# Kernel tuning notes

Measured on AMD Instinct MI355X. Metric: run time of the kernel, lower is better.

The kernel has to match this reference:

```python
import jax, jax.numpy as jnp
import numpy as np

D_MODEL = 1024
HEADS = 16
HEAD_DIM = D_MODEL // HEADS
SEQ_LEN = 2048
BATCH = 2
LN_EPS = 1e-5


def _layernorm(x, gamma, beta):
    mu = jnp.mean(x, axis=-1, keepdims=True)
    var = jnp.var(x, axis=-1, keepdims=True)
    return (x - mu) * jax.lax.rsqrt(var + LN_EPS) * gamma + beta


def setup_inputs() -> dict:
    key = jax.random.key(0)
    ks = jax.random.split(key, 12)
    d, h = D_MODEL, 4 * D_MODEL
    s = lambda fan_in: 1.0 / np.sqrt(fan_in)
    return {
        "x": jax.random.normal(ks[0], (BATCH, SEQ_LEN, d), dtype=jnp.float32),
        "W_qkv": jax.random.uniform(ks[1], (d, 3 * d), minval=-s(d), maxval=s(d)),
        "b_qkv": jax.random.uniform(ks[2], (3 * d,), minval=-s(d), maxval=s(d)),
        "W1": jax.random.uniform(ks[3], (d, h), minval=-s(d), maxval=s(d)),
        "b1": jax.random.uniform(ks[4], (h,), minval=-s(d), maxval=s(d)),
        "W2": jax.random.uniform(ks[5], (h, d), minval=-s(h), maxval=s(h)),
        "b2": jax.random.uniform(ks[6], (d,), minval=-s(h), maxval=s(h)),
        "ln1_g": jnp.ones((d,), jnp.float32),
        "ln1_b": jnp.zeros((d,), jnp.float32),
        "ln2_g": jnp.ones((d,), jnp.float32),
        "ln2_b": jnp.zeros((d,), jnp.float32),
    }


def reference(x, W_qkv, b_qkv, W1, b1, W2, b2, ln1_g, ln1_b, ln2_g, ln2_b):
    B, T, C = x.shape
    # QKV projection -> [B, T, 3, H, hs] -> q,k,v each [B, H, T, hs]
    qkv = (x @ W_qkv + b_qkv).reshape(B, T, 3, HEADS, HEAD_DIM)
    qkv = jnp.transpose(qkv, (2, 0, 3, 1, 4))
    q, k, v = qkv[0], qkv[1], qkv[2]
    # Naive causal attention with full [B,H,T,T] score matrix (matches source)
    A = jnp.einsum("bhqd,bhkd->bhqk", q, k) / jnp.sqrt(jnp.float32(HEAD_DIM))
    causal = jnp.tril(jnp.ones((T, T), dtype=bool))
    A = jnp.where(causal, A, -jnp.inf)
    A = jax.nn.softmax(A, axis=-1)
    attn = jnp.einsum("bhqk,bhkd->bhqd", A, v)  # [B,H,T,hs]
    attn = jnp.transpose(attn, (0, 2, 1, 3)).reshape(B, T, C)
    # Residual + LN, FFN, residual + LN (dropout=0 / eval)
    h = _layernorm(x + attn, ln1_g, ln1_b)
    ff = jax.nn.relu(h @ W1 + b1) @ W2 + b2
    return _layernorm(h + ff, ln2_g, ln2_b)
```

## Files before the change

### kernel.cpp

```cpp
#include <hip/hip_runtime.h>

#define D_MODEL 1024
#define HEADS   16
#define HEAD_DIM 64
#define SEQ     2048
#define BATCH   2
#define ROWS    (BATCH*SEQ)
#define FFDIM   4096

typedef __attribute__((ext_vector_type(8))) short short8;
typedef __attribute__((ext_vector_type(4))) float f32x4;
typedef __attribute__((ext_vector_type(4))) unsigned short us4;

typedef const __attribute__((address_space(1))) unsigned int* gptr_t;
typedef __attribute__((address_space(3))) unsigned int* lptr_t;

__device__ __forceinline__ unsigned short f2bf(float f){
  unsigned int x = __float_as_uint(f);
  x += 0x7fffu + ((x >> 16) & 1u);
  return (unsigned short)(x >> 16);
}

__device__ __forceinline__ float wave_sum(float x){
  #pragma unroll
  for (int off = 32; off; off >>= 1) x += __shfl_xor(x, off);
  return x;
}

__global__ __launch_bounds__(256) void cast_bf16_kernel(const float* __restrict__ in,
                                                        unsigned short* __restrict__ out, int n4){
  int i = blockIdx.x * 256 + threadIdx.x;
  if (i >= n4) return;
  float4 v = *(const float4*)(in + (size_t)i * 4);
  us4 o;
  o[0] = f2bf(v.x); o[1] = f2bf(v.y); o[2] = f2bf(v.z); o[3] = f2bf(v.w);
  *(us4*)(out + (size_t)i * 4) = o;
}

__global__ __launch_bounds__(256) void transpose_cast_kernel(const float* __restrict__ in,
                                                             unsigned short* __restrict__ out,
                                                             int R, int C){
  __shared__ float tile[32][33];
  const int bc = blockIdx.x * 32, br = blockIdx.y * 32;
  const int tx = threadIdx.x & 31, ty = threadIdx.x >> 5;
  #pragma unroll
  for (int j = 0; j < 4; ++j)
    tile[ty + 8*j][tx] = in[(size_t)(br + ty + 8*j) * C + bc + tx];
  __syncthreads();
  #pragma unroll
  for (int j = 0; j < 4; ++j)
    out[(size_t)(bc + ty + 8*j) * R + br + tx] = f2bf(tile[tx][ty + 8*j]);
}

template<int EPI>
__global__ __launch_bounds__(256) void gemm_kernel(const unsigned short* __restrict__ A,
                                                   const unsigned short* __restrict__ BT,
                                                   const float* __restrict__ bias,
                                                   int M, int N, int K, int kchunk,
                                                   int gx, int gy,
                                                   float* __restrict__ outF,
                                                   unsigned short* __restrict__ outH,
                                                   unsigned short* __restrict__ qo,
                                                   unsigned short* __restrict__ ko,
                                                   unsigned short* __restrict__ vT){
  __shared__ __align__(16) unsigned short Alds[2][128 * 32];
  __shared__ __align__(16) unsigned short Blds[2][128 * 32];
  const int tid = threadIdx.x;
  const int lane = tid & 63;
  const int wid = tid >> 6;
  const int wr = wid >> 1, wc = wid & 1;
  const int lrow = lane & 15, lgrp = lane >> 4;

  const int nwg = gridDim.x;
  const int cpx = nwg >> 3;
  const int wg = (blockIdx.x & 7) * cpx + (blockIdx.x >> 3);
  const int nx = wg % gx;
  const int rest = wg / gx;
  const int my = rest % gy;
  const int sk = rest / gy;

  const int m0 = my * 128, n0 = nx * 128;
  const int kbase0 = sk * kchunk;

  const int sr = lane >> 2, sc = (lane & 3) * 8;

  f32x4 acc[4][4];
  #pragma unroll
  for (int i = 0; i < 4; ++i)
    #pragma unroll
    for (int j = 0; j < 4; ++j)
      acc[i][j] = f32x4{0.f, 0.f, 0.f, 0.f};

  #pragma unroll
  for (int it = 0; it < 2; ++it){
    const int c = wid * 2 + it;
    const int r = c * 16 + sr;
    __builtin_amdgcn_global_load_lds(
        (gptr_t)(const void*)(A + (size_t)(m0 + r) * K + kbase0 + sc),
        (lptr_t)(void*)(&Alds[0][c * 512]), 16, 0, 0);
    __builtin_amdgcn_global_load_lds(
        (gptr_t)(const void*)(BT + (size_t)(n0 + r) * K + kbase0 + sc),
        (lptr_t)(void*)(&Blds[0][c * 512]), 16, 0, 0);
  }

  const int nk = kchunk >> 5;
  int cur = 0;
  for (int kt = 0; kt < nk; ++kt){
    __syncthreads();

    if (kt + 1 < nk){
      const int kb = kbase0 + (kt + 1) * 32;
      #pragma unroll
      for (int it = 0; it < 2; ++it){
        const int c = wid * 2 + it;
        const int r = c * 16 + sr;
        __builtin_amdgcn_global_load_lds(
            (gptr_t)(const void*)(A + (size_t)(m0 + r) * K + kb + sc),
            (lptr_t)(void*)(&Alds[cur ^ 1][c * 512]), 16, 0, 0);
        __builtin_amdgcn_global_load_lds(
            (gptr_t)(const void*)(BT + (size_t)(n0 + r) * K + kb + sc),
            (lptr_t)(void*)(&Blds[cur ^ 1][c * 512]), 16, 0, 0);
      }
    }

    short8 af[4], bfr[4];
    #pragma unroll
    for (int f = 0; f < 4; ++f){
      af[f]  = *(const short8*)&Alds[cur][(wr * 64 + f * 16 + lrow) * 32 + lgrp * 8];
      bfr[f] = *(const short8*)&Blds[cur][(wc * 64 + f * 16 + lrow) * 32 + lgrp * 8];
    }
    __builtin_amdgcn_s_setprio(1);
    #pragma unroll
    for (int i = 0; i < 4; ++i)
      #pragma unroll
      for (int j = 0; j < 4; ++j)
        acc[i][j] = __builtin_amdgcn_mfma_f32_16x16x32_bf16(af[i], bfr[j], acc[i][j], 0, 0, 0);
    __builtin_amdgcn_s_setprio(0);
    cur ^= 1;
  }

  float* const outP = (EPI == 3) ? outF + (size_t)sk * M * N : outF;
  #pragma unroll
  for (int i = 0; i < 4; ++i){
    const int rg = m0 + wr * 64 + i * 16 + lgrp * 4;
    #pragma unroll
    for (int j = 0; j < 4; ++j){
      const int cg = n0 + wc * 64 + j * 16 + lrow;
      const float bb = (EPI == 3) ? 0.f : bias[cg];
      if constexpr (EPI == 0){
        const int which = cg >> 10, rem = cg & 1023;
        const int hh = rem >> 6, dd = rem & 63;
        const int bb_ = rg >> 11, tt = rg & 2047;
        const size_t bh = (size_t)(bb_ * HEADS + hh);
        if (which == 2){
          us4 pk;
          #pragma unroll
          for (int r = 0; r < 4; ++r) pk[r] = f2bf(acc[i][j][r] + bb);
          *(us4*)(vT + (bh * 64 + dd) * SEQ + tt) = pk;
        } else {
          unsigned short* dst = which ? ko : qo;
          const float sc2 = which ? 1.0f : 0.18033688f;
          #pragma unroll
          for (int r = 0; r < 4; ++r)
            dst[(bh * SEQ + tt + r) * 64 + dd] = f2bf((acc[i][j][r] + bb) * sc2);
        }
      } else if constexpr (EPI == 1){
        #pragma unroll
        for (int r = 0; r < 4; ++r)
          outH[(size_t)(rg + r) * N + cg] = f2bf(fmaxf(acc[i][j][r] + bb, 0.f));
      } else {
        #pragma unroll
        for (int r = 0; r < 4; ++r)
          outP[(size_t)(rg + r) * N + cg] = acc[i][j][r] + bb;
      }
    }
  }
}

__global__ __launch_bounds__(512, 2) void gemm256_kernel(const unsigned short* __restrict__ A,
                                                         const unsigned short* __restrict__ BT,
                                                         const float* __restrict__ bias,
                                                         int M, int N, int K, int gx,
                                                         unsigned short* __restrict__ outH){
  __shared__ __align__(16) unsigned short Al[2][256 * 32];
  __shared__ __align__(16) unsigned short Bl[2][256 * 32];
  const int tid = threadIdx.x;
  const int lane = tid & 63;
  const int wid = tid >> 6;
  const int wm = wid >> 2, wn = wid & 3;
  const int lr = lane & 15, g = lane >> 4;

  const int nwg = gridDim.x;
  const int cpx = nwg >> 3;
  const int wg = (blockIdx.x & 7) * cpx + (blockIdx.x >> 3);
  const int nx = wg % gx, my = wg / gx;
  const int m0 = my * 256, n0 = nx * 256;

  f32x4 acc[8][4];
  #pragma unroll
  for (int i = 0; i < 8; ++i)
    #pragma unroll
    for (int j = 0; j < 4; ++j)
      acc[i][j] = f32x4{0.f, 0.f, 0.f, 0.f};

  auto STAGE = [&](int buf, int kt){
    const int kb = kt * 32;
    #pragma unroll
    for (int j = 0; j < 2; ++j){
      const int cc = tid + j * 512;
      const int row = cc >> 2, c = cc & 3;
      const int scol = ((c ^ (row & 3)) << 3);
      __builtin_amdgcn_global_load_lds(
          (gptr_t)(const void*)(A + (size_t)(m0 + row) * K + kb + scol),
          (lptr_t)(void*)(&Al[buf][cc * 8]), 16, 0, 0);
      __builtin_amdgcn_global_load_lds(
          (gptr_t)(const void*)(BT + (size_t)(n0 + row) * K + kb + scol),
          (lptr_t)(void*)(&Bl[buf][cc * 8]), 16, 0, 0);
    }
  };

  const int nk = K >> 5;
  STAGE(0, 0);
  for (int t = 0; t < nk; ++t){
    const int buf = t & 1;
    __syncthreads();
    if (t + 1 < nk) STAGE(buf ^ 1, t + 1);

    short8 af[8], bf[4];
    #pragma unroll
    for (int i = 0; i < 8; ++i){
      const int row = wm * 128 + i * 16 + lr;
      af[i] = *(const short8*)&Al[buf][row * 32 + ((g * 8) ^ ((row & 3) << 3))];
    }
    #pragma unroll
    for (int j = 0; j < 4; ++j){
      const int row = wn * 64 + j * 16 + lr;
      bf[j] = *(const short8*)&Bl[buf][row * 32 + ((g * 8) ^ ((row & 3) << 3))];
    }
    __builtin_amdgcn_s_setprio(1);
    #pragma unroll
    for (int i = 0; i < 8; ++i)
      #pragma unroll
      for (int j = 0; j < 4; ++j)
        acc[i][j] = __builtin_amdgcn_mfma_f32_16x16x32_bf16(af[i], bf[j], acc[i][j], 0, 0, 0);
    __builtin_amdgcn_s_setprio(0);
  }

  #pragma unroll
  for (int i = 0; i < 8; ++i){
    const int rg = m0 + wm * 128 + i * 16 + g * 4;
    #pragma unroll
    for (int j = 0; j < 4; ++j){
      const int cg = n0 + wn * 64 + j * 16 + lr;
      const float bb = bias[cg];
      #pragma unroll
      for (int r = 0; r < 4; ++r)
        outH[(size_t)(rg + r) * N + cg] = f2bf(fmaxf(acc[i][j][r] + bb, 0.f));
    }
  }
}

__global__ __launch_bounds__(256) void attn_mfma_kernel(const unsigned short* __restrict__ Qb,
                                                        const unsigned short* __restrict__ Kb,
                                                        const unsigned short* __restrict__ VT,
                                                        float* __restrict__ Op){
  __shared__ __align__(16) char Kl[2][8192];
  __shared__ __align__(16) char Vl[2][8192];
  __shared__ __align__(16) char Pl[4][4096];
  const int tid = threadIdx.x;
  const int w = tid >> 6, lane = tid & 63;
  const int lr = lane & 15, g = lane >> 4;

  const int bx = blockIdx.x, u = bx & 255, half = bx >> 8;
  const int g8 = u >> 5;
  const int qg = half ? g8 : 15 - g8;
  const int bh = u & 31;

  const int q0w = qg * 128 + w * 32;
  const int qA = q0w + lr, qB = qA + 16;

  const char* const KbB = (const char*)(Kb + (size_t)bh * SEQ * 64);
  const char* const VbB = (const char*)(VT + (size_t)bh * 64 * SEQ);
  char* const PbA = Pl[w];
  char* const PbB = Pl[w] + 2048;

  const unsigned short* qra = Qb + ((size_t)bh * SEQ + qA) * 64 + g * 8;
  const short8 qfA0 = *(const short8*)(qra);
  const short8 qfA1 = *(const short8*)(qra + 32);
  const short8 qfB0 = *(const short8*)(qra + 16 * 64);
  const short8 qfB1 = *(const short8*)(qra + 16 * 64 + 32);

  f32x4 oA[4], oB[4];
  #pragma unroll
  for (int dt = 0; dt < 4; ++dt){ oA[dt] = f32x4{0.f,0.f,0.f,0.f}; oB[dt] = f32x4{0.f,0.f,0.f,0.f}; }
  float lA = 0.f, lB = 0.f;
  const int swzl = (lr & 7) << 4;

  const int kbmax = 2 * qg + 1;

  short8 st[4];
  {
    #pragma unroll
    for (int c = 0; c < 2; ++c){
      const int L = c * 4096 + tid * 16;
      st[c] = *(const short8*)(KbB + L);
      const int row = L >> 7, col = L & 127;
      st[2 + c] = *(const short8*)(VbB + (size_t)row * 4096 + col);
    }
  }

  for (int kb = 0; kb <= kbmax; ++kb){
    const int p = kb & 1;
    const int k0 = kb * 64;

    #pragma unroll
    for (int c = 0; c < 2; ++c){
      const int L = c * 4096 + tid * 16;
      const int row = L >> 7, col = L & 127;
      const int dst = row * 128 + (col ^ ((row & 7) << 4));
      *(short8*)(Kl[p] + dst) = st[c];
      *(short8*)(Vl[p] + dst) = st[2 + c];
    }
    __syncthreads();

    if (kb < kbmax){
      #pragma unroll
      for (int c = 0; c < 2; ++c){
        const int L = c * 4096 + tid * 16;
        st[c] = *(const short8*)(KbB + (size_t)(kb + 1) * 8192 + L);
        const int row = L >> 7, col = L & 127;
        st[2 + c] = *(const short8*)(VbB + (size_t)row * 4096 + (size_t)(kb + 1) * 128 + col);
      }
    }

    f32x4 sA[4], sB[4];
    __builtin_amdgcn_s_setprio(1);
    #pragma unroll
    for (int kt = 0; kt < 4; ++kt){
      const int row = kt * 16 + lr;
      const int ro = row * 128, sw = (row & 7) << 4;
      const short8 kf0 = *(const short8*)(Kl[p] + ro + ((g * 16) ^ sw));
      const short8 kf1 = *(const short8*)(Kl[p] + ro + ((64 + g * 16) ^ sw));
      sA[kt] = __builtin_amdgcn_mfma_f32_16x16x32_bf16(kf0, qfA0, f32x4{0.f,0.f,0.f,0.f}, 0, 0, 0);
      sA[kt] = __builtin_amdgcn_mfma_f32_16x16x32_bf16(kf1, qfA1, sA[kt], 0, 0, 0);
      sB[kt] = __builtin_amdgcn_mfma_f32_16x16x32_bf16(kf0, qfB0, f32x4{0.f,0.f,0.f,0.f}, 0, 0, 0);
      sB[kt] = __builtin_amdgcn_mfma_f32_16x16x32_bf16(kf1, qfB1, sB[kt], 0, 0, 0);
    }
    __builtin_amdgcn_s_setprio(0);

    if (kb >= kbmax - 1){
      #pragma unroll
      for (int kt = 0; kt < 4; ++kt)
        #pragma unroll
        for (int r = 0; r < 4; ++r){
          const int key = k0 + kt * 16 + g * 4 + r;
          if (key > qA) sA[kt][r] = -INFINITY;
          if (key > qB) sB[kt][r] = -INFINITY;
        }
    }

    {
      float sum = 0.f;
      #pragma unroll
      for (int kt = 0; kt < 4; ++kt){
        #pragma unroll
        for (int r = 0; r < 4; ++r){
          const float pp = __builtin_amdgcn_exp2f(sA[kt][r]);
          sA[kt][r] = pp; sum += pp;
        }
        unsigned int p01, p23;
        asm("v_cvt_pk_bf16_f32 %0, %1, %2" : "=v"(p01) : "v"(sA[kt][0]), "v"(sA[kt][1]));
        asm("v_cvt_pk_bf16_f32 %0, %1, %2" : "=v"(p23) : "v"(sA[kt][2]), "v"(sA[kt][3]));
        uint2 pk; pk.x = p01; pk.y = p23;
        *(uint2*)(PbA + lr * 128 + ((kt * 32 + g * 8) ^ swzl)) = pk;
      }
      sum += __shfl_xor(sum, 16);
      sum += __shfl_xor(sum, 32);
      lA += sum;
    }
    {
      float sum = 0.f;
      #pragma unroll
      for (int kt = 0; kt < 4; ++kt){
        #pragma unroll
        for (int r = 0; r < 4; ++r){
          const float pp = __builtin_amdgcn_exp2f(sB[kt][r]);
          sB[kt][r] = pp; sum += pp;
        }
        unsigned int p01, p23;
        asm("v_cvt_pk_bf16_f32 %0, %1, %2" : "=v"(p01) : "v"(sB[kt][0]), "v"(sB[kt][1]));
        asm("v_cvt_pk_bf16_f32 %0, %1, %2" : "=v"(p23) : "v"(sB[kt][2]), "v"(sB[kt][3]));
        uint2 pk; pk.x = p01; pk.y = p23;
        *(uint2*)(PbB + lr * 128 + ((kt * 32 + g * 8) ^ swzl)) = pk;
      }
      sum += __shfl_xor(sum, 16);
      sum += __shfl_xor(sum, 32);
      lB += sum;
    }

    const short8 paA0 = *(const short8*)(PbA + lr * 128 + ((g * 16) ^ swzl));
    const short8 paA1 = *(const short8*)(PbA + lr * 128 + ((64 + g * 16) ^ swzl));
    const short8 paB0 = *(const short8*)(PbB + lr * 128 + ((g * 16) ^ swzl));
    const short8 paB1 = *(const short8*)(PbB + lr * 128 + ((64 + g * 16) ^ swzl));
    __builtin_amdgcn_s_setprio(1);
    #pragma unroll
    for (int dt = 0; dt < 4; ++dt){
      const int row = dt * 16 + lr;
      const int ro = row * 128, sw = (row & 7) << 4;
      const short8 vf0 = *(const short8*)(Vl[p] + ro + ((g * 16) ^ sw));
      const short8 vf1 = *(const short8*)(Vl[p] + ro + ((64 + g * 16) ^ sw));
      oA[dt] = __builtin_amdgcn_mfma_f32_16x16x32_bf16(paA0, vf0, oA[dt], 0, 0, 0);
      oA[dt] = __builtin_amdgcn_mfma_f32_16x16x32_bf16(paA1, vf1, oA[dt], 0, 0, 0);
      oB[dt] = __builtin_amdgcn_mfma_f32_16x16x32_bf16(paB0, vf0, oB[dt], 0, 0, 0);
      oB[dt] = __builtin_amdgcn_mfma_f32_16x16x32_bf16(paB1, vf1, oB[dt], 0, 0, 0);
    }
    __builtin_amdgcn_s_setprio(0);
  }

  const int b = bh >> 4, hh = bh & 15;
  {
    float lv[4];
    #pragma unroll
    for (int r = 0; r < 4; ++r) lv[r] = __shfl(lA, g * 4 + r);
    #pragma unroll
    for (int dt = 0; dt < 4; ++dt)
      #pragma unroll
      for (int r = 0; r < 4; ++r)
        Op[((size_t)(b * SEQ) + q0w + g * 4 + r) * D_MODEL + hh * 64 + dt * 16 + lr] = oA[dt][r] / lv[r];
  }
  {
    float lv[4];
    #pragma unroll
    for (int r = 0; r < 4; ++r) lv[r] = __shfl(lB, g * 4 + r);
    #pragma unroll
    for (int dt = 0; dt < 4; ++dt)
      #pragma unroll
      for (int r = 0; r < 4; ++r)
        Op[((size_t)(b * SEQ) + q0w + 16 + g * 4 + r) * D_MODEL + hh * 64 + dt * 16 + lr] = oB[dt][r] / lv[r];
  }
}

__global__ __launch_bounds__(256) void ln_kernel(const float* __restrict__ A,
                                                 const float* __restrict__ B1,
                                                 const float* __restrict__ B2,
                                                 const float* __restrict__ bias,
                                                 const float* __restrict__ g,
                                                 const float* __restrict__ be,
                                                 float* __restrict__ outF,
                                                 unsigned short* __restrict__ outH){
  const int row = blockIdx.x, tid = threadIdx.x;
  const size_t base = (size_t)row * D_MODEL + tid * 4;
  float4 va = *(const float4*)(A + base);
  float4 vb = *(const float4*)(B1 + base);
  float v0 = va.x + vb.x, v1 = va.y + vb.y, v2 = va.z + vb.z, v3 = va.w + vb.w;
  if (B2){
    float4 vc = *(const float4*)(B2 + base);
    v0 += vc.x; v1 += vc.y; v2 += vc.z; v3 += vc.w;
  }
  if (bias){
    float4 vd = *(const float4*)(bias + tid * 4);
    v0 += vd.x; v1 += vd.y; v2 += vd.z; v3 += vd.w;
  }
  float s  = v0 + v1 + v2 + v3;
  float ss = v0*v0 + v1*v1 + v2*v2 + v3*v3;
  s = wave_sum(s); ss = wave_sum(ss);
  __shared__ float red[8];
  const int w = tid >> 6, lane = tid & 63;
  if (!lane){ red[w] = s; red[4 + w] = ss; }
  __syncthreads();
  s  = red[0] + red[1] + red[2] + red[3];
  ss = red[4] + red[5] + red[6] + red[7];
  const float mu  = s * (1.0f / D_MODEL);
  const float var = ss * (1.0f / D_MODEL) - mu * mu;
  const float rstd = rsqrtf(var + 1e-5f);
  float4 gg = *(const float4*)(g  + tid * 4);
  float4 bb = *(const float4*)(be + tid * 4);
  const float r0 = (v0 - mu) * rstd * gg.x + bb.x;
  const float r1 = (v1 - mu) * rstd * gg.y + bb.y;
  const float r2 = (v2 - mu) * rstd * gg.z + bb.z;
  const float r3 = (v3 - mu) * rstd * gg.w + bb.w;
  float4 of; of.x = r0; of.y = r1; of.z = r2; of.w = r3;
  *(float4*)(outF + base) = of;
  if (outH){
    us4 oh; oh[0] = f2bf(r0); oh[1] = f2bf(r1); oh[2] = f2bf(r2); oh[3] = f2bf(r3);
    *(us4*)(outH + base) = oh;
  }
}

extern "C" void kernel_launch(void* const* d_in, const int* in_sizes, int n_in,
                              void* d_out, int out_size, void* d_ws, size_t ws_size,
                              hipStream_t stream){
  (void)in_sizes; (void)n_in; (void)out_size;
  const float* x     = (const float*)d_in[0];
  const float* W_qkv = (const float*)d_in[1];
  const float* b_qkv = (const float*)d_in[2];
  const float* W1    = (const float*)d_in[3];
  const float* b1    = (const float*)d_in[4];
  const float* W2    = (const float*)d_in[5];
  const float* b2    = (const float*)d_in[6];
  const float* ln1g  = (const float*)d_in[7];
  const float* ln1b  = (const float*)d_in[8];
  const float* ln2g  = (const float*)d_in[9];
  const float* ln2b  = (const float*)d_in[10];

  char* ws = (char*)d_ws;
  const size_t MB = 1024ull * 1024ull;
  unsigned short* WqkvT = (unsigned short*)(ws + 0 * MB);
  unsigned short* W1T   = (unsigned short*)(ws + 6 * MB);
  unsigned short* W2T   = (unsigned short*)(ws + 14 * MB);
  unsigned short* xbf   = (unsigned short*)(ws + 22 * MB);
  unsigned short* qB    = (unsigned short*)(ws + 30 * MB);
  unsigned short* kB    = (unsigned short*)(ws + 39 * MB);
  unsigned short* vT    = (unsigned short*)(ws + 48 * MB);
  float* attn = (float*)(ws + 57 * MB);
  float* hF           = (float*)(ws + 30 * MB);
  unsigned short* hB  = (unsigned short*)(ws + 46 * MB);
  unsigned short* ff1 = (unsigned short*)(ws + 54 * MB);
  float* p0           = (float*)(ws + 86 * MB);
  float* p1           = (float*)(ws + 102 * MB);

  const int nsplit = (ws_size >= 119 * MB) ? 2 : 1;

  cast_bf16_kernel<<<4096, 256, 0, stream>>>(x, xbf, ROWS * D_MODEL / 4);
  transpose_cast_kernel<<<dim3(96, 32), 256, 0, stream>>>(W_qkv, WqkvT, 1024, 3072);
  transpose_cast_kernel<<<dim3(128, 32), 256, 0, stream>>>(W1, W1T, 1024, 4096);
  transpose_cast_kernel<<<dim3(32, 128), 256, 0, stream>>>(W2, W2T, 4096, 1024);

  gemm_kernel<0><<<768, 256, 0, stream>>>(
      xbf, WqkvT, b_qkv, ROWS, 3072, 1024, 1024, 24, 32, nullptr, nullptr, qB, kB, vT);

  attn_mfma_kernel<<<512, 256, 0, stream>>>(qB, kB, vT, attn);

  ln_kernel<<<ROWS, 256, 0, stream>>>(x, attn, nullptr, nullptr, ln1g, ln1b, hF, hB);

  gemm256_kernel<<<256, 512, 0, stream>>>(
      hB, W1T, b1, ROWS, FFDIM, 1024, 16, ff1);

  gemm_kernel<3><<<256 * nsplit, 256, 0, stream>>>(
      ff1, W2T, nullptr, ROWS, 1024, FFDIM, FFDIM / nsplit, 8, 32, p0, nullptr, nullptr, nullptr, nullptr);

  ln_kernel<<<ROWS, 256, 0, stream>>>(hF, p0, (nsplit == 2) ? p1 : nullptr, b2,
                                      ln2g, ln2b, (float*)d_out, nullptr);
}
```

Before: 218.9 us.

## Add 256x256 eight-phase pipelined GEMM for all projections with bf16 split-K partials

Replaces the 128x128 QKV GEMM and the 256-tile FFN1 GEMM with a new 512-thread 256x256 kernel. It uses a four-buffer LDS ring with 64-wide K steps, XOR-swizzled layout, and interleaved phases of fragment loads, MFMAs and barriers with fine-grained vmcnt waits. The FFN2 GEMM now uses 4-way split-K with bf16 partials that the final layernorm sums. This is meant to raise MFMA utilisation and cut partial-sum traffic, at the cost of extra precision loss from bf16 partials and fewer workgroups for the QKV GEMM.

```diff
diff --git a/kernel.cpp b/kernel.cpp
--- a/kernel.cpp
+++ b/kernel.cpp
@@ -53,101 +53,154 @@
 }
 
 template<int EPI>
-__global__ __launch_bounds__(256) void gemm_kernel(const unsigned short* __restrict__ A,
-                                                   const unsigned short* __restrict__ BT,
-                                                   const float* __restrict__ bias,
-                                                   int M, int N, int K, int kchunk,
-                                                   int gx, int gy,
-                                                   float* __restrict__ outF,
-                                                   unsigned short* __restrict__ outH,
-                                                   unsigned short* __restrict__ qo,
-                                                   unsigned short* __restrict__ ko,
-                                                   unsigned short* __restrict__ vT){
-  __shared__ __align__(16) unsigned short Alds[2][128 * 32];
-  __shared__ __align__(16) unsigned short Blds[2][128 * 32];
-  const int tid = threadIdx.x;
-  const int lane = tid & 63;
-  const int wid = tid >> 6;
-  const int wr = wid >> 1, wc = wid & 1;
-  const int lrow = lane & 15, lgrp = lane >> 4;
-
-  const int nwg = gridDim.x;
-  const int cpx = nwg >> 3;
+__global__ __launch_bounds__(512, 1) void gemm8p_kernel(const unsigned short* __restrict__ A,
+                                                        const unsigned short* __restrict__ BT,
+                                                        const float* __restrict__ bias,
+                                                        int M, int N, int K, int kchunk,
+                                                        int gx, int gy,
+                                                        unsigned short* __restrict__ outH,
+                                                        unsigned short* __restrict__ qo,
+                                                        unsigned short* __restrict__ ko,
+                                                        unsigned short* __restrict__ vT){
+  __shared__ __align__(16) unsigned short Ab[2][2][256 * 32];
+  __shared__ __align__(16) unsigned short Bb[2][2][256 * 32];
+  const int tid = threadIdx.x, lane = tid & 63, wid = tid >> 6;
+  const int wm = wid >> 2, wn = wid & 3;
+  const int lr = lane & 15, g = lane >> 4;
+
+  const int nwg = gridDim.x, cpx = nwg >> 3;
   const int wg = (blockIdx.x & 7) * cpx + (blockIdx.x >> 3);
   const int nx = wg % gx;
   const int rest = wg / gx;
   const int my = rest % gy;
   const int sk = rest / gy;
-
-  const int m0 = my * 128, n0 = nx * 128;
-  const int kbase0 = sk * kchunk;
-
-  const int sr = lane >> 2, sc = (lane & 3) * 8;
-
-  f32x4 acc[4][4];
-  #pragma unroll
-  for (int i = 0; i < 4; ++i)
+  const int m0 = my * 256, n0 = nx * 256, kb0 = sk * kchunk;
+  const int nk = kchunk >> 6;
+
+  f32x4 acc[8][4];
+  #pragma unroll
+  for (int i = 0; i < 8; ++i)
     #pragma unroll
     for (int j = 0; j < 4; ++j)
       acc[i][j] = f32x4{0.f, 0.f, 0.f, 0.f};
 
-  #pragma unroll
-  for (int it = 0; it < 2; ++it){
-    const int c = wid * 2 + it;
-    const int r = c * 16 + sr;
-    __builtin_amdgcn_global_load_lds(
-        (gptr_t)(const void*)(A + (size_t)(m0 + r) * K + kbase0 + sc),
-        (lptr_t)(void*)(&Alds[0][c * 512]), 16, 0, 0);
-    __builtin_amdgcn_global_load_lds(
-        (gptr_t)(const void*)(BT + (size_t)(n0 + r) * K + kbase0 + sc),
-        (lptr_t)(void*)(&Blds[0][c * 512]), 16, 0, 0);
-  }
-
-  const int nk = kchunk >> 5;
-  int cur = 0;
-  for (int kt = 0; kt < nk; ++kt){
-    __syncthreads();
-
-    if (kt + 1 < nk){
-      const int kb = kbase0 + (kt + 1) * 32;
-      #pragma unroll
-      for (int it = 0; it < 2; ++it){
-        const int c = wid * 2 + it;
-        const int r = c * 16 + sr;
-        __builtin_amdgcn_global_load_lds(
-            (gptr_t)(const void*)(A + (size_t)(m0 + r) * K + kb + sc),
-            (lptr_t)(void*)(&Alds[cur ^ 1][c * 512]), 16, 0, 0);
-        __builtin_amdgcn_global_load_lds(
-            (gptr_t)(const void*)(BT + (size_t)(n0 + r) * K + kb + sc),
-            (lptr_t)(void*)(&Blds[cur ^ 1][c * 512]), 16, 0, 0);
-      }
-    }
-
-    short8 af[4], bfr[4];
-    #pragma unroll
-    for (int f = 0; f < 4; ++f){
-      af[f]  = *(const short8*)&Alds[cur][(wr * 64 + f * 16 + lrow) * 32 + lgrp * 8];
-      bfr[f] = *(const short8*)&Blds[cur][(wc * 64 + f * 16 + lrow) * 32 + lgrp * 8];
-    }
+  auto STAGE = [&](int op, int t, int kh){
+    const int d = t & 1;
+    unsigned short* base = op ? &Bb[d][kh][0] : &Ab[d][kh][0];
+    const unsigned short* src = op ? BT : A;
+    const int r0 = op ? n0 : m0;
+    #pragma unroll
+    for (int j = 0; j < 2; ++j){
+      const int L = tid + j * 512;
+      const int row = L >> 2, c = L & 3;
+      __builtin_amdgcn_global_load_lds(
+          (gptr_t)(const void*)(src + (size_t)(r0 + row) * K + kb0 + t * 64 + kh * 32
+                                + ((c ^ ((row >> 1) & 3)) << 3)),
+          (lptr_t)(void*)(base + L * 8), 16, 0, 0);
+    }
+  };
+
+  STAGE(0,0,0); STAGE(1,0,0); STAGE(0,0,1); STAGE(1,0,1);
+  STAGE(0,1,0); STAGE(1,1,0); STAGE(0,1,1); STAGE(1,1,1);
+  asm volatile("s_waitcnt vmcnt(8)" ::: "memory");
+  __builtin_amdgcn_s_barrier();
+
+  short8 afr[8], bfr[4];
+
+  #define PHASE_SYNC(T)                                              \
+    if ((T) < 2)              asm volatile("s_waitcnt vmcnt(4)" ::: "memory"); \
+    else if ((T) <= nk - 3)   asm volatile("s_waitcnt vmcnt(8)" ::: "memory"); \
+    else                      asm volatile("s_waitcnt vmcnt(0)" ::: "memory"); \
+    __builtin_amdgcn_s_barrier();                                    \
+    asm volatile("s_waitcnt lgkmcnt(0)" ::: "memory");               \
+    __builtin_amdgcn_sched_barrier(0);
+
+  for (int t = 0; t < nk; ++t){
+    const int d = t & 1;
+    #pragma unroll
+    for (int i = 0; i < 8; ++i){
+      const int row = wm * 128 + i * 16 + lr;
+      afr[i] = *(const short8*)&Ab[d][0][row * 32 + ((g ^ ((row >> 1) & 3)) << 3)];
+    }
+    #pragma unroll
+    for (int j = 0; j < 2; ++j){
+      const int row = wn * 64 + j * 16 + lr;
+      bfr[j] = *(const short8*)&Bb[d][0][row * 32 + ((g ^ ((row >> 1) & 3)) << 3)];
+    }
+    if (t >= 1 && t + 1 < nk) STAGE(1, t + 1, 1);
+    PHASE_SYNC(t)
     __builtin_amdgcn_s_setprio(1);
     #pragma unroll
-    for (int i = 0; i < 4; ++i)
-      #pragma unroll
-      for (int j = 0; j < 4; ++j)
-        acc[i][j] = __builtin_amdgcn_mfma_f32_16x16x32_bf16(af[i], bfr[j], acc[i][j], 0, 0, 0);
+    for (int i = 0; i < 8; ++i){
+      acc[i][0] = __builtin_amdgcn_mfma_f32_16x16x32_bf16(afr[i], bfr[0], acc[i][0], 0, 0, 0);
+      acc[i][1] = __builtin_amdgcn_mfma_f32_16x16x32_bf16(afr[i], bfr[1], acc[i][1], 0, 0, 0);
+    }
     __builtin_amdgcn_s_setprio(0);
-    cur ^= 1;
-  }
-
-  float* const outP = (EPI == 3) ? outF + (size_t)sk * M * N : outF;
-  #pragma unroll
-  for (int i = 0; i < 4; ++i){
-    const int rg = m0 + wr * 64 + i * 16 + lgrp * 4;
+    __builtin_amdgcn_s_barrier();
+
+    #pragma unroll
+    for (int j = 0; j < 2; ++j){
+      const int row = wn * 64 + (2 + j) * 16 + lr;
+      bfr[2 + j] = *(const short8*)&Bb[d][0][row * 32 + ((g ^ ((row >> 1) & 3)) << 3)];
+    }
+    if (t + 2 < nk) STAGE(0, t + 2, 0);
+    PHASE_SYNC(t)
+    __builtin_amdgcn_s_setprio(1);
+    #pragma unroll
+    for (int i = 0; i < 8; ++i){
+      acc[i][2] = __builtin_amdgcn_mfma_f32_16x16x32_bf16(afr[i], bfr[2], acc[i][2], 0, 0, 0);
+      acc[i][3] = __builtin_amdgcn_mfma_f32_16x16x32_bf16(afr[i], bfr[3], acc[i][3], 0, 0, 0);
+    }
+    __builtin_amdgcn_s_setprio(0);
+    __builtin_amdgcn_s_barrier();
+
+    #pragma unroll
+    for (int i = 0; i < 8; ++i){
+      const int row = wm * 128 + i * 16 + lr;
+      afr[i] = *(const short8*)&Ab[d][1][row * 32 + ((g ^ ((row >> 1) & 3)) << 3)];
+    }
+    #pragma unroll
+    for (int j = 0; j < 2; ++j){
+      const int row = wn * 64 + j * 16 + lr;
+      bfr[j] = *(const short8*)&Bb[d][1][row * 32 + ((g ^ ((row >> 1) & 3)) << 3)];
+    }
+    if (t + 2 < nk) STAGE(1, t + 2, 0);
+    PHASE_SYNC(t)
+    __builtin_amdgcn_s_setprio(1);
+    #pragma unroll
+    for (int i = 0; i < 8; ++i){
+      acc[i][0] = __builtin_amdgcn_mfma_f32_16x16x32_bf16(afr[i], bfr[0], acc[i][0], 0, 0, 0);
+      acc[i][1] = __builtin_amdgcn_mfma_f32_16x16x32_bf16(afr[i], bfr[1], acc[i][1], 0, 0, 0);
+    }
+    __builtin_amdgcn_s_setprio(0);
+    __builtin_amdgcn_s_barrier();
+
+    #pragma unroll
+    for (int j = 0; j < 2; ++j){
+      const int row = wn * 64 + (2 + j) * 16 + lr;
+      bfr[2 + j] = *(const short8*)&Bb[d][1][row * 32 + ((g ^ ((row >> 1) & 3)) << 3)];
+    }
+    if (t + 2 < nk) STAGE(0, t + 2, 1);
+    PHASE_SYNC(t)
+    __builtin_amdgcn_s_setprio(1);
+    #pragma unroll
+    for (int i = 0; i < 8; ++i){
+      acc[i][2] = __builtin_amdgcn_mfma_f32_16x16x32_bf16(afr[i], bfr[2], acc[i][2], 0, 0, 0);
+      acc[i][3] = __builtin_amdgcn_mfma_f32_16x16x32_bf16(afr[i], bfr[3], acc[i][3], 0, 0, 0);
+    }
+    __builtin_amdgcn_s_setprio(0);
+    __builtin_amdgcn_s_barrier();
+  }
+  #undef PHASE_SYNC
+
+  #pragma unroll
+  for (int i = 0; i < 8; ++i){
+    const int rg = m0 + wm * 128 + i * 16 + g * 4;
     #pragma unroll
     for (int j = 0; j < 4; ++j){
-      const int cg = n0 + wc * 64 + j * 16 + lrow;
-      const float bb = (EPI == 3) ? 0.f : bias[cg];
+      const int cg = n0 + wn * 64 + j * 16 + lr;
       if constexpr (EPI == 0){
+        const float bb = bias[cg];
         const int which = cg >> 10, rem = cg & 1023;
         const int hh = rem >> 6, dd = rem & 63;
         const int bb_ = rg >> 11, tt = rg & 2047;
@@ -165,99 +218,112 @@
             dst[(bh * SEQ + tt + r) * 64 + dd] = f2bf((acc[i][j][r] + bb) * sc2);
         }
       } else if constexpr (EPI == 1){
+        const float bb = bias[cg];
         #pragma unroll
         for (int r = 0; r < 4; ++r)
           outH[(size_t)(rg + r) * N + cg] = f2bf(fmaxf(acc[i][j][r] + bb, 0.f));
       } else {
+        unsigned short* dst = outH + (size_t)sk * M * N;
         #pragma unroll
         for (int r = 0; r < 4; ++r)
-          outP[(size_t)(rg + r) * N + cg] = acc[i][j][r] + bb;
+          dst[(size_t)(rg + r) * N + cg] = f2bf(acc[i][j][r]);
       }
     }
   }
 }
 
-__global__ __launch_bounds__(512, 2) void gemm256_kernel(const unsigned short* __restrict__ A,
-                                                         const unsigned short* __restrict__ BT,
-                                                         const float* __restrict__ bias,
-                                                         int M, int N, int K, int gx,
-                                                         unsigned short* __restrict__ outH){
-  __shared__ __align__(16) unsigned short Al[2][256 * 32];
-  __shared__ __align__(16) unsigned short Bl[2][256 * 32];
+template<int EPI>
+__global__ __launch_bounds__(256) void gemm_kernel(const unsigned short* __restrict__ A,
+                                                   const unsigned short* __restrict__ BT,
+                                                   const float* __restrict__ bias,
+                                                   int M, int N, int K, int kchunk,
+                                                   int gx, int gy,
+                                                   float* __restrict__ outF,
+                                                   unsigned short* __restrict__ outH){
+  __shared__ __align__(16) unsigned short Alds[2][128 * 32];
+  __shared__ __align__(16) unsigned short Blds[2][128 * 32];
   const int tid = threadIdx.x;
   const int lane = tid & 63;
   const int wid = tid >> 6;
-  const int wm = wid >> 2, wn = wid & 3;
-  const int lr = lane & 15, g = lane >> 4;
+  const int wr = wid >> 1, wc = wid & 1;
+  const int lrow = lane & 15, lgrp = lane >> 4;
 
   const int nwg = gridDim.x;
   const int cpx = nwg >> 3;
   const int wg = (blockIdx.x & 7) * cpx + (blockIdx.x >> 3);
-  const int nx = wg % gx, my = wg / gx;
-  const int m0 = my * 256, n0 = nx * 256;
-
-  f32x4 acc[8][4];
-  #pragma unroll
-  for (int i = 0; i < 8; ++i)
+  const int nx = wg % gx;
+  const int rest = wg / gx;
+  const int my = rest % gy;
+  const int sk = rest / gy;
+
+  const int m0 = my * 128, n0 = nx * 128;
+  const int kbase0 = sk * kchunk;
+  const int sr = lane >> 2, sc = (lane & 3) * 8;
+
+  f32x4 acc[4][4];
+  #pragma unroll
+  for (int i = 0; i < 4; ++i)
     #pragma unroll
     for (int j = 0; j < 4; ++j)
       acc[i][j] = f32x4{0.f, 0.f, 0.f, 0.f};
 
-  auto STAGE = [&](int buf, int kt){
-    const int kb = kt * 32;
-    #pragma unroll
-    for (int j = 0; j < 2; ++j){
-      const int cc = tid + j * 512;
-      const int row = cc >> 2, c = cc & 3;
-      const int scol = ((c ^ (row & 3)) << 3);
-      __builtin_amdgcn_global_load_lds(
-          (gptr_t)(const void*)(A + (size_t)(m0 + row) * K + kb + scol),
-          (lptr_t)(void*)(&Al[buf][cc * 8]), 16, 0, 0);
-      __builtin_amdgcn_global_load_lds(
-          (gptr_t)(const void*)(BT + (size_t)(n0 + row) * K + kb + scol),
-          (lptr_t)(void*)(&Bl[buf][cc * 8]), 16, 0, 0);
-    }
-  };
-
-  const int nk = K >> 5;
-  STAGE(0, 0);
-  for (int t = 0; t < nk; ++t){
-    const int buf = t & 1;
+  #pragma unroll
+  for (int it = 0; it < 2; ++it){
+    const int c = wid * 2 + it;
+    const int r = c * 16 + sr;
+    __builtin_amdgcn_global_load_lds(
+        (gptr_t)(const void*)(A + (size_t)(m0 + r) * K + kbase0 + sc),
+        (lptr_t)(void*)(&Alds[0][c * 512]), 16, 0, 0);
+    __builtin_amdgcn_global_load_lds(
+        (gptr_t)(const void*)(BT + (size_t)(n0 + r) * K + kbase0 + sc),
+        (lptr_t)(void*)(&Blds[0][c * 512]), 16, 0, 0);
+  }
+
+  const int nk = kchunk >> 5;
+  int cur = 0;
+  for (int kt = 0; kt < nk; ++kt){
     __syncthreads();
-    if (t + 1 < nk) STAGE(buf ^ 1, t + 1);
-
-    short8 af[8], bf[4];
-    #pragma unroll
-    for (int i = 0; i < 8; ++i){
-      const int row = wm * 128 + i * 16 + lr;
-      af[i] = *(const short8*)&Al[buf][row * 32 + ((g * 8) ^ ((row & 3) << 3))];
-    }
+    if (kt + 1 < nk){
+      const int kb = kbase0 + (kt + 1) * 32;
+      #pragma unroll
+      for (int it = 0; it < 2; ++it){
+        const int c = wid * 2 + it;
+        const int r = c * 16 + sr;
+        __builtin_amdgcn_global_load_lds(
+            (gptr_t)(const void*)(A + (size_t)(m0 + r) * K + kb + sc),
+            (lptr_t)(void*)(&Alds[cur ^ 1][c * 512]), 16, 0, 0);
+        __builtin_amdgcn_global_load_lds(
+            (gptr_t)(const void*)(BT + (size_t)(n0 + r) * K + kb + sc),
+            (lptr_t)(void*)(&Blds[cur ^ 1][c * 512]), 16, 0, 0);
+      }
+    }
+    short8 af[4], bfr[4];
+    #pragma unroll
+    for (int f = 0; f < 4; ++f){
+      af[f]  = *(const short8*)&Alds[cur][(wr * 64 + f * 16 + lrow) * 32 + lgrp * 8];
+      bfr[f] = *(const short8*)&Blds[cur][(wc * 64 + f * 16 + lrow) * 32 + lgrp * 8];
+    }
+    #pragma unroll
+    for (int i = 0; i < 4; ++i)
+      #pragma unroll
+      for (int j = 0; j < 4; ++j)
+        acc[i][j] = __builtin_amdgcn_mfma_f32_16x16x32_bf16(af[i], bfr[j], acc[i][j], 0, 0, 0);
+    cur ^= 1;
+  }
+
+  float* const outP = outF + (size_t)sk * M * N;
+  #pragma unroll
+  for (int i = 0; i < 4; ++i){
+    const int rg = m0 + wr * 64 + i * 16 + lgrp * 4;
     #pragma unroll
     for (int j = 0; j < 4; ++j){
-      const int row = wn * 64 + j * 16 + lr;
-      bf[j] = *(const short8*)&Bl[buf][row * 32 + ((g * 8) ^ ((row & 3) << 3))];
-    }
-    __builtin_amdgcn_s_setprio(1);
-    #pragma unroll
-    for (int i = 0; i < 8; ++i)
-      #pragma unroll
-      for (int j = 0; j < 4; ++j)
-        acc[i][j] = __builtin_amdgcn_mfma_f32_16x16x32_bf16(af[i], bf[j], acc[i][j], 0, 0, 0);
-    __builtin_amdgcn_s_setprio(0);
-  }
-
-  #pragma unroll
-  for (int i = 0; i < 8; ++i){
-    const int rg = m0 + wm * 128 + i * 16 + g * 4;
-    #pragma unroll
-    for (int j = 0; j < 4; ++j){
-      const int cg = n0 + wn * 64 + j * 16 + lr;
-      const float bb = bias[cg];
+      const int cg = n0 + wc * 64 + j * 16 + lrow;
       #pragma unroll
       for (int r = 0; r < 4; ++r)
-        outH[(size_t)(rg + r) * N + cg] = f2bf(fmaxf(acc[i][j][r] + bb, 0.f));
-    }
-  }
+        outP[(size_t)(rg + r) * N + cg] = acc[i][j][r];
+    }
+  }
+  (void)bias; (void)outH;
 }
 
 __global__ __launch_bounds__(256) void attn_mfma_kernel(const unsigned short* __restrict__ Qb,
@@ -442,7 +508,8 @@
 
 __global__ __launch_bounds__(256) void ln_kernel(const float* __restrict__ A,
                                                  const float* __restrict__ B1,
-                                                 const float* __restrict__ B2,
+                                                 const unsigned short* __restrict__ P4,
+                                                 size_t pstride,
                                                  const float* __restrict__ bias,
                                                  const float* __restrict__ g,
                                                  const float* __restrict__ be,
@@ -451,11 +518,20 @@
   const int row = blockIdx.x, tid = threadIdx.x;
   const size_t base = (size_t)row * D_MODEL + tid * 4;
   float4 va = *(const float4*)(A + base);
-  float4 vb = *(const float4*)(B1 + base);
-  float v0 = va.x + vb.x, v1 = va.y + vb.y, v2 = va.z + vb.z, v3 = va.w + vb.w;
-  if (B2){
-    float4 vc = *(const float4*)(B2 + base);
-    v0 += vc.x; v1 += vc.y; v2 += vc.z; v3 += vc.w;
+  float v0 = va.x, v1 = va.y, v2 = va.z, v3 = va.w;
+  if (B1){
+    float4 vb = *(const float4*)(B1 + base);
+    v0 += vb.x; v1 += vb.y; v2 += vb.z; v3 += vb.w;
+  }
+  if (P4){
+    #pragma unroll
+    for (int p = 0; p < 4; ++p){
+      us4 u = *(const us4*)(P4 + p * pstride + base);
+      v0 += __uint_as_float((unsigned int)u[0] << 16);
+      v1 += __uint_as_float((unsigned int)u[1] << 16);
+      v2 += __uint_as_float((unsigned int)u[2] << 16);
+      v3 += __uint_as_float((unsigned int)u[3] << 16);
+    }
   }
   if (bias){
     float4 vd = *(const float4*)(bias + tid * 4);
@@ -487,6 +563,41 @@
   }
 }
 
+__global__ __launch_bounds__(256) void ln2f_kernel(const float* __restrict__ A,
+                                                   const float* __restrict__ B1,
+                                                   const float* __restrict__ bias,
+                                                   const float* __restrict__ g,
+                                                   const float* __restrict__ be,
+                                                   float* __restrict__ outF){
+  const int row = blockIdx.x, tid = threadIdx.x;
+  const size_t base = (size_t)row * D_MODEL + tid * 4;
+  float4 va = *(const float4*)(A + base);
+  float4 vb = *(const float4*)(B1 + base);
+  float4 vd = *(const float4*)(bias + tid * 4);
+  float v0 = va.x + vb.x + vd.x, v1 = va.y + vb.y + vd.y;
+  float v2 = va.z + vb.z + vd.z, v3 = va.w + vb.w + vd.w;
+  float s  = v0 + v1 + v2 + v3;
+  float ss = v0*v0 + v1*v1 + v2*v2 + v3*v3;
+  s = wave_sum(s); ss = wave_sum(ss);
+  __shared__ float red[8];
+  const int w = tid >> 6, lane = tid & 63;
+  if (!lane){ red[w] = s; red[4 + w] = ss; }
+  __syncthreads();
+  s  = red[0] + red[1] + red[2] + red[3];
+  ss = red[4] + red[5] + red[6] + red[7];
+  const float mu  = s * (1.0f / D_MODEL);
+  const float var = ss * (1.0f / D_MODEL) - mu * mu;
+  const float rstd = rsqrtf(var + 1e-5f);
+  float4 gg = *(const float4*)(g  + tid * 4);
+  float4 bb = *(const float4*)(be + tid * 4);
+  float4 of;
+  of.x = (v0 - mu) * rstd * gg.x + bb.x;
+  of.y = (v1 - mu) * rstd * gg.y + bb.y;
+  of.z = (v2 - mu) * rstd * gg.z + bb.z;
+  of.w = (v3 - mu) * rstd * gg.w + bb.w;
+  *(float4*)(outF + base) = of;
+}
+
 extern "C" void kernel_launch(void* const* d_in, const int* in_sizes, int n_in,
                               void* d_out, int out_size, void* d_ws, size_t ws_size,
                               hipStream_t stream){
@@ -516,29 +627,34 @@
   float* hF           = (float*)(ws + 30 * MB);
   unsigned short* hB  = (unsigned short*)(ws + 46 * MB);
   unsigned short* ff1 = (unsigned short*)(ws + 54 * MB);
+  unsigned short* pbf = (unsigned short*)(ws + 86 * MB);
   float* p0           = (float*)(ws + 86 * MB);
-  float* p1           = (float*)(ws + 102 * MB);
-
-  const int nsplit = (ws_size >= 119 * MB) ? 2 : 1;
+
+  const int use8p = (ws_size >= 118 * MB);
 
   cast_bf16_kernel<<<4096, 256, 0, stream>>>(x, xbf, ROWS * D_MODEL / 4);
   transpose_cast_kernel<<<dim3(96, 32), 256, 0, stream>>>(W_qkv, WqkvT, 1024, 3072);
   transpose_cast_kernel<<<dim3(128, 32), 256, 0, stream>>>(W1, W1T, 1024, 4096);
   transpose_cast_kernel<<<dim3(32, 128), 256, 0, stream>>>(W2, W2T, 4096, 1024);
 
-  gemm_kernel<0><<<768, 256, 0, stream>>>(
-      xbf, WqkvT, b_qkv, ROWS, 3072, 1024, 1024, 24, 32, nullptr, nullptr, qB, kB, vT);
+  gemm8p_kernel<0><<<192, 512, 0, stream>>>(
+      xbf, WqkvT, b_qkv, ROWS, 3072, 1024, 1024, 12, 16, nullptr, qB, kB, vT);
 
   attn_mfma_kernel<<<512, 256, 0, stream>>>(qB, kB, vT, attn);
 
-  ln_kernel<<<ROWS, 256, 0, stream>>>(x, attn, nullptr, nullptr, ln1g, ln1b, hF, hB);
-
-  gemm256_kernel<<<256, 512, 0, stream>>>(
-      hB, W1T, b1, ROWS, FFDIM, 1024, 16, ff1);
-
-  gemm_kernel<3><<<256 * nsplit, 256, 0, stream>>>(
-      ff1, W2T, nullptr, ROWS, 1024, FFDIM, FFDIM / nsplit, 8, 32, p0, nullptr, nullptr, nullptr, nullptr);
-
-  ln_kernel<<<ROWS, 256, 0, stream>>>(hF, p0, (nsplit == 2) ? p1 : nullptr, b2,
-                                      ln2g, ln2b, (float*)d_out, nullptr);
-}
+  ln_kernel<<<ROWS, 256, 0, stream>>>(x, attn, nullptr, 0, nullptr, ln1g, ln1b, hF, hB);
+
+  gemm8p_kernel<1><<<256, 512, 0, stream>>>(
+      hB, W1T, b1, ROWS, FFDIM, 1024, 1024, 16, 16, ff1, nullptr, nullptr, nullptr);
+
+  if (use8p){
+    gemm8p_kernel<4><<<256, 512, 0, stream>>>(
+        ff1, W2T, nullptr, ROWS, 1024, FFDIM, 1024, 4, 16, pbf, nullptr, nullptr, nullptr);
+    ln_kernel<<<ROWS, 256, 0, stream>>>(hF, nullptr, pbf, (size_t)ROWS * 1024, b2,
+                                        ln2g, ln2b, (float*)d_out, nullptr);
+  } else {
+    gemm_kernel<3><<<256, 256, 0, stream>>>(
+        ff1, W2T, nullptr, ROWS, 1024, FFDIM, FFDIM, 8, 32, p0, nullptr);
+    ln2f_kernel<<<ROWS, 256, 0, stream>>>(hF, p0, b2, ln2g, ln2b, (float*)d_out);
+  }
+}
```

Result: faster. 206.2 us (-5.8%).
